# Performance work log

Measured on AMD Instinct MI355X. Metric: run time of the kernel, lower is better.

The kernel has to match this reference:

```python
import jax, jax.numpy as jnp
import numpy as np

NUM_IDS = 100000
DIM = 128
NODE_COUNT = 50000
NB_COUNT = 32


def setup_inputs() -> dict:
    key = jax.random.key(0)
    k1, k2 = jax.random.split(key)
    neighs = jax.random.randint(k1, (NODE_COUNT * NB_COUNT,), 0, NUM_IDS, dtype=jnp.int64 if jax.config.jax_enable_x64 else jnp.int32)
    emb_table = jax.random.normal(k2, (NUM_IDS, DIM), dtype=jnp.float32)
    return {"neighs": neighs, "node_count": NODE_COUNT, "emb_table": emb_table}


def reference(neighs, node_count, emb_table):
    # features(neighs): gather rows of the embedding table  -> [node_count*nb_count, d]
    neigh_feats = emb_table[neighs]
    nb_count = neigh_feats.shape[0] // node_count
    # view(node_count, nb_count, d).sum(1)
    fv_by_node = neigh_feats.reshape(node_count, nb_count, neigh_feats.shape[-1])
    return fv_by_node.sum(axis=1)
```

## Files before the change

### kernel.cpp

```cpp
#include <hip/hip_runtime.h>
#include <hip/hip_bf16.h>
#include <hip/hip_fp16.h>


constexpr int DIM = 128;
constexpr int DIM4 = DIM / 4;
constexpr int NB = 32;

__global__ __launch_bounds__(256) void convert_kernel(
    const float4* __restrict__ emb,
    uint2* __restrict__ emb_h,
    int n4)
{
    int i = blockIdx.x * blockDim.x + threadIdx.x;
    int stride = gridDim.x * blockDim.x;
    for (; i < n4; i += stride) {
        float4 v = emb[i];
        __half2 h0 = __floats2half2_rn(v.x, v.y);
        __half2 h1 = __floats2half2_rn(v.z, v.w);
        uint2 o;
        o.x = *reinterpret_cast<unsigned int*>(&h0);
        o.y = *reinterpret_cast<unsigned int*>(&h1);
        emb_h[i] = o;
    }
}

__global__ __launch_bounds__(256) void gather_h_kernel(
    const int* __restrict__ neighs,
    const uint2* __restrict__ emb_h,
    float4* __restrict__ out,
    int node_count)
{
    int t = blockIdx.x * blockDim.x + threadIdx.x;
    int node = t >> 5;
    int lane = t & 31;
    if (node >= node_count) return;

    int my_idx = neighs[node * NB + lane];

    float4 acc = make_float4(0.f, 0.f, 0.f, 0.f);
#pragma unroll 8
    for (int i = 0; i < NB; ++i) {
        int id = __shfl(my_idx, i, 32);
        uint2 u = emb_h[(size_t)id * DIM4 + lane];
        __half2 p0 = *reinterpret_cast<__half2*>(&u.x);
        __half2 p1 = *reinterpret_cast<__half2*>(&u.y);
        float2 f0 = __half22float2(p0);
        float2 f1 = __half22float2(p1);
        acc.x += f0.x; acc.y += f0.y; acc.z += f1.x; acc.w += f1.y;
    }
    out[(size_t)node * DIM4 + lane] = acc;
}

__global__ __launch_bounds__(256) void gather_f32_kernel(
    const int* __restrict__ neighs,
    const float4* __restrict__ emb,
    float4* __restrict__ out,
    int node_count, int nb_count)
{
    int t = blockIdx.x * blockDim.x + threadIdx.x;
    int node = t >> 5;
    int lane = t & 31;
    if (node >= node_count) return;

    const int* __restrict__ idx = neighs + (size_t)node * nb_count;
    float4 acc = make_float4(0.f, 0.f, 0.f, 0.f);
    for (int i = 0; i < nb_count; ++i) {
        int id = idx[i];
        float4 v = emb[(size_t)id * DIM4 + lane];
        acc.x += v.x; acc.y += v.y; acc.z += v.z; acc.w += v.w;
    }
    out[(size_t)node * DIM4 + lane] = acc;
}

extern "C" void kernel_launch(void* const* d_in, const int* in_sizes, int n_in,
                              void* d_out, int out_size, void* d_ws, size_t ws_size,
                              hipStream_t stream)
{
    const int* neighs = (const int*)d_in[0];
    const float4* emb = (const float4*)d_in[2];
    float4* out = (float4*)d_out;

    const int node_count = out_size / DIM;
    const int nb_count   = in_sizes[0] / node_count;
    const int num_ids    = in_sizes[2] / DIM;

    const size_t ws_needed = (size_t)num_ids * DIM * sizeof(__half);

    const int block = 256;

    if (nb_count == NB && ws_size >= ws_needed) {
        uint2* emb_h = (uint2*)d_ws;
        const int n4 = num_ids * DIM4;
        convert_kernel<<<2048, block, 0, stream>>>(emb, emb_h, n4);

        const int threads_total = node_count * 32;
        const int grid = (threads_total + block - 1) / block;
        gather_h_kernel<<<grid, block, 0, stream>>>(neighs, emb_h, out, node_count);
    } else {
        const int threads_total = node_count * 32;
        const int grid = (threads_total + block - 1) / block;
        gather_f32_kernel<<<grid, block, 0, stream>>>(neighs, emb, out, node_count, nb_count);
    }
}
```

Baseline: 148.0 us.

## Bucket-sort neighbor ids per node and gather 8 nodes per wavefront

Adds a prep kernel that reorders each node's 32 neighbor ids by table region (id >> 13) using wave ballots. The gather is reworked so each 64-lane wave handles 8 nodes, with each lane reading one half2 of a row. All 8 nodes step through their sorted neighbors together, which is meant to keep concurrent row reads inside a narrower slice of the fp16 table for better cache locality and more memory-level parallelism. This costs an extra kernel launch and a round trip of the index array through global memory. The convert kernel also switches from a grid-stride loop to one element per thread.

```diff
diff --git a/kernel.cpp b/kernel.cpp
--- a/kernel.cpp
+++ b/kernel.cpp
@@ -4,8 +4,10 @@
 
 
 constexpr int DIM = 128;
-constexpr int DIM4 = DIM / 4;
 constexpr int NB = 32;
+constexpr int SHIFT = 13;
+
+typedef float floatx4 __attribute__((ext_vector_type(4)));
 
 __global__ __launch_bounds__(256) void convert_kernel(
     const float4* __restrict__ emb,
@@ -13,43 +15,89 @@
     int n4)
 {
     int i = blockIdx.x * blockDim.x + threadIdx.x;
-    int stride = gridDim.x * blockDim.x;
-    for (; i < n4; i += stride) {
-        float4 v = emb[i];
-        __half2 h0 = __floats2half2_rn(v.x, v.y);
-        __half2 h1 = __floats2half2_rn(v.z, v.w);
-        uint2 o;
-        o.x = *reinterpret_cast<unsigned int*>(&h0);
-        o.y = *reinterpret_cast<unsigned int*>(&h1);
-        emb_h[i] = o;
-    }
+    if (i >= n4) return;
+    float4 v = emb[i];
+    __half2 h0 = __floats2half2_rn(v.x, v.y);
+    __half2 h1 = __floats2half2_rn(v.z, v.w);
+    uint2 o;
+    o.x = *reinterpret_cast<unsigned int*>(&h0);
+    o.y = *reinterpret_cast<unsigned int*>(&h1);
+    emb_h[i] = o;
 }
 
-__global__ __launch_bounds__(256) void gather_h_kernel(
+__global__ __launch_bounds__(256) void prep_kernel(
     const int* __restrict__ neighs,
-    const uint2* __restrict__ emb_h,
-    float4* __restrict__ out,
+    int* __restrict__ sorted,
+    int node_count, int nr)
+{
+    const int t    = threadIdx.x;
+    const int ln   = t & 31;
+    const int half = (t >> 5) & 1;
+    const int node = blockIdx.x * 8 + (t >> 5);
+    if (node >= node_count) return;
+
+    int my_idx = neighs[(size_t)node * NB + ln];
+    int my_r   = my_idx >> SHIFT;
+
+    const unsigned int below = (1u << ln) - 1u;
+    int cum = 0, pos = 0;
+    for (int r = 0; r < nr; ++r) {
+        bool hit = (my_r == r);
+        unsigned long long b = __ballot(hit);
+        unsigned int gb = (unsigned int)(b >> (half * 32));
+        if (hit) pos = cum + __popc(gb & below);
+        cum += __popc(gb);
+    }
+    sorted[(size_t)node * NB + pos] = my_idx;
+}
+
+__global__ __launch_bounds__(256) void gather_sorted(
+    const unsigned int* __restrict__ tbl,
+    const int* __restrict__ sorted,
+    float2* __restrict__ out,
     int node_count)
 {
-    int t = blockIdx.x * blockDim.x + threadIdx.x;
-    int node = t >> 5;
-    int lane = t & 31;
-    if (node >= node_count) return;
+    const int lane  = threadIdx.x & 63;
+    const int wave  = threadIdx.x >> 6;
+    const int node0 = blockIdx.x * 32 + wave * 8;
 
-    int my_idx = neighs[node * NB + lane];
+    int nc8[8];
+#pragma unroll
+    for (int ln = 0; ln < 8; ++ln) {
+        int n = node0 + ln;
+        nc8[ln] = (n < node_count) ? n : (node_count - 1);
+    }
 
-    float4 acc = make_float4(0.f, 0.f, 0.f, 0.f);
-#pragma unroll 8
-    for (int i = 0; i < NB; ++i) {
-        int id = __shfl(my_idx, i, 32);
-        uint2 u = emb_h[(size_t)id * DIM4 + lane];
-        __half2 p0 = *reinterpret_cast<__half2*>(&u.x);
-        __half2 p1 = *reinterpret_cast<__half2*>(&u.y);
-        float2 f0 = __half22float2(p0);
-        float2 f1 = __half22float2(p1);
-        acc.x += f0.x; acc.y += f0.y; acc.z += f1.x; acc.w += f1.y;
+    float2 acc[8];
+#pragma unroll
+    for (int ln = 0; ln < 8; ++ln) acc[ln] = make_float2(0.f, 0.f);
+
+    for (int k = 0; k < NB; ++k) {
+        int id[8];
+#pragma unroll
+        for (int ln = 0; ln < 8; ++ln)
+            id[ln] = sorted[(size_t)nc8[ln] * NB + k];
+
+        unsigned int u[8];
+#pragma unroll
+        for (int ln = 0; ln < 8; ++ln)
+            u[ln] = tbl[(size_t)id[ln] * 64 + lane];
+
+#pragma unroll
+        for (int ln = 0; ln < 8; ++ln) {
+            __half2 h = *reinterpret_cast<__half2*>(&u[ln]);
+            float2 f = __half22float2(h);
+            acc[ln].x += f.x;
+            acc[ln].y += f.y;
+        }
     }
-    out[(size_t)node * DIM4 + lane] = acc;
+
+#pragma unroll
+    for (int ln = 0; ln < 8; ++ln) {
+        int n = node0 + ln;
+        if (n < node_count)
+            out[(size_t)n * 64 + lane] = acc[ln];
+    }
 }
 
 __global__ __launch_bounds__(256) void gather_f32_kernel(
@@ -67,10 +115,10 @@
     float4 acc = make_float4(0.f, 0.f, 0.f, 0.f);
     for (int i = 0; i < nb_count; ++i) {
         int id = idx[i];
-        float4 v = emb[(size_t)id * DIM4 + lane];
+        float4 v = emb[(size_t)id * (DIM / 4) + lane];
         acc.x += v.x; acc.y += v.y; acc.z += v.z; acc.w += v.w;
     }
-    out[(size_t)node * DIM4 + lane] = acc;
+    out[(size_t)node * (DIM / 4) + lane] = acc;
 }
 
 extern "C" void kernel_launch(void* const* d_in, const int* in_sizes, int n_in,
@@ -79,27 +127,34 @@
 {
     const int* neighs = (const int*)d_in[0];
     const float4* emb = (const float4*)d_in[2];
-    float4* out = (float4*)d_out;
 
     const int node_count = out_size / DIM;
     const int nb_count   = in_sizes[0] / node_count;
     const int num_ids    = in_sizes[2] / DIM;
 
-    const size_t ws_needed = (size_t)num_ids * DIM * sizeof(__half);
+    const size_t tbl_bytes = (size_t)num_ids * DIM * sizeof(__half);
+    const size_t ws_needed = tbl_bytes + (size_t)node_count * NB * 4;
 
     const int block = 256;
 
     if (nb_count == NB && ws_size >= ws_needed) {
-        uint2* emb_h = (uint2*)d_ws;
-        const int n4 = num_ids * DIM4;
-        convert_kernel<<<2048, block, 0, stream>>>(emb, emb_h, n4);
+        unsigned int* tbl_h = (unsigned int*)d_ws;
+        int* sorted = (int*)((char*)d_ws + tbl_bytes);
+        const int nr = (num_ids + (1 << SHIFT) - 1) >> SHIFT;
 
-        const int threads_total = node_count * 32;
-        const int grid = (threads_total + block - 1) / block;
-        gather_h_kernel<<<grid, block, 0, stream>>>(neighs, emb_h, out, node_count);
+        const int n4 = num_ids * (DIM / 4);
+        convert_kernel<<<(n4 + block - 1) / block, block, 0, stream>>>(
+            emb, (uint2*)tbl_h, n4);
+
+        prep_kernel<<<(node_count + 7) / 8, block, 0, stream>>>(
+            neighs, sorted, node_count, nr);
+
+        gather_sorted<<<(node_count + 31) / 32, block, 0, stream>>>(
+            tbl_h, sorted, (float2*)d_out, node_count);
     } else {
         const int threads_total = node_count * 32;
         const int grid = (threads_total + block - 1) / block;
-        gather_f32_kernel<<<grid, block, 0, stream>>>(neighs, emb, out, node_count, nb_count);
+        gather_f32_kernel<<<grid, block, 0, stream>>>(
+            neighs, emb, (float4*)d_out, node_count, nb_count);
     }
 }
```

Result: slower. 159.2 us (+7.6%).
